# Kernel tuning notes

Measured on AMD Instinct MI355X. Metric: run time of the kernel, lower is better.

Reference implementation:

```python
import jax, jax.numpy as jnp
import numpy as np
import math

N = 4096      # n_history
D = 512       # embed_dim
H = 8         # time-weight MLP hidden size


def setup_inputs() -> dict:
    key = jax.random.key(0)
    k1, k2, k3, k4, k5 = jax.random.split(key, 5)
    return {
        "query_code_embeds": jax.random.normal(k1, (N, D), dtype=jnp.float32),
        "hist_embeddings": jax.random.normal(k2, (N, D), dtype=jnp.float32),
        "hist_times": jax.random.uniform(k3, (N,), dtype=jnp.float32),
        "tw_w1": jax.random.normal(k4, (1, H), dtype=jnp.float32) * (1.0 / math.sqrt(1.0)),
        "tw_b1": jnp.zeros((H,), dtype=jnp.float32),
        "tw_w2": jax.random.normal(k5, (H, 1), dtype=jnp.float32) * (1.0 / math.sqrt(H)),
        "tw_b2": jnp.zeros((1,), dtype=jnp.float32),
    }


def reference(query_code_embeds, hist_embeddings, hist_times, tw_w1, tw_b1, tw_w2, tw_b2):
    # pairwise absolute time differences: [n, n, 1]
    time_diffs = jnp.abs(hist_times[:, None] - hist_times[None, :])[..., None]
    # pointwise MLP on time diffs -> multiplicative attention bias [n, n]
    h = jax.nn.relu(time_diffs @ tw_w1 + tw_b1)            # [n, n, H]
    time_weights = jax.nn.sigmoid(h @ tw_w2 + tw_b2)[..., 0]  # [n, n]
    # scaled dot-product scores modulated by time weights
    scores = (query_code_embeds @ hist_embeddings.T) / math.sqrt(D)
    scores = scores * time_weights
    attn = jax.nn.softmax(scores, axis=1)
    return attn @ hist_embeddings
```

## Files before the change

### kernel.cpp

```cpp
#include <hip/hip_runtime.h>
#include <hip/hip_cooperative_groups.h>

namespace cg = cooperative_groups;

#define N 4096
#define D 512
#define FRAG_SH 512
#define NBLK 512
#define NTHR 256
#define SC_STRIDE 136
#define SMEM_BYTES 69632

typedef __attribute__((ext_vector_type(8))) short short8;
typedef __attribute__((ext_vector_type(4))) float f32x4;

__device__ __forceinline__ unsigned short f2bf(float f) {
    unsigned int u = __float_as_uint(f);
    u = (u + 0x7FFFu + ((u >> 16) & 1u)) >> 16;
    return (unsigned short)u;
}
__device__ __forceinline__ unsigned short f2bf_rn(float f) {
    return (unsigned short)((__float_as_uint(f) + 0x8000u) >> 16);
}
__device__ __forceinline__ float bf2f(unsigned short u) {
    return __uint_as_float((unsigned)u << 16);
}

__device__ __forceinline__ void prep_phase(int bid, int tid,
    const float* __restrict__ q, const float* __restrict__ hist,
    unsigned short* __restrict__ Qblk, unsigned short* __restrict__ Kblk,
    unsigned short* __restrict__ Vblk, float* __restrict__ dsum)
{
    extern __shared__ unsigned short smem[];
    if (bid >= 256) {
        if (bid < 258) {
            int z = (bid - 256) * NTHR + tid;
            #pragma unroll
            for (int j = 0; j < 8; ++j) dsum[z * 8 + j] = 0.f;
        }
        return;
    }
    const bool isQ = bid < 128;
    const int t = isQ ? bid : bid - 128;
    const float* src = isQ ? q : hist;
    const float scale = isQ ? 0.04419417382415922f : 1.0f;

    #pragma unroll
    for (int k = 0; k < 16; ++k) {
        int idx = tid + k * 256;
        int row = idx >> 7;
        int c4  = (idx & 127) << 2;
        float4 v = *(const float4*)(src + (size_t)(t * 32 + row) * D + c4);
        ushort4 o;
        o.x = f2bf(v.x * scale); o.y = f2bf(v.y * scale);
        o.z = f2bf(v.z * scale); o.w = f2bf(v.w * scale);
        *(ushort4*)(smem + row * 512 + c4) = o;
    }
    __syncthreads();

    unsigned short* ABdst = isQ ? Qblk : Kblk;
    #pragma unroll
    for (int k = 0; k < 8; ++k) {
        int s = tid + k * 256;
        int fl = s >> 6, ln = s & 63;
        int dk = fl >> 1, rbl = fl & 1;
        int l16 = ln & 15, qq = ln >> 4;
        short8 v = *(const short8*)(smem + (rbl * 16 + l16) * 512 + dk * 32 + qq * 8);
        *(short8*)(ABdst + ((size_t)dk * 256 + t * 2 + rbl) * FRAG_SH + ln * 8) = v;
    }
    if (!isQ) {
        #pragma unroll
        for (int k = 0; k < 8; ++k) {
            int s = tid + k * 256;
            int db = s >> 6, ln = s & 63;
            int l16 = ln & 15, qq = ln >> 4;
            unsigned short tmp[8];
            #pragma unroll
            for (int j = 0; j < 8; ++j)
                tmp[j] = smem[(qq * 8 + j) * 512 + db * 16 + l16];
            *(short8*)(Vblk + ((size_t)t * 32 + db) * FRAG_SH + ln * 8) = *(const short8*)tmp;
        }
    }
}

__device__ __forceinline__ void qk_phase(int bid, int tid,
    const unsigned short* __restrict__ Qblk, const unsigned short* __restrict__ Kblk,
    const float* __restrict__ times,
    const float* __restrict__ w1, const float* __restrict__ b1,
    const float* __restrict__ w2, const float* __restrict__ b2,
    unsigned short* __restrict__ Pblk, float* __restrict__ dsum)
{
    extern __shared__ unsigned short smem[];
    const int wv = tid >> 6, lane = tid & 63;
    const int qq = lane >> 4, l16 = lane & 15;
    const int wy = wv >> 1, wx = wv & 1;
    const int rg = bid >> 4;
    const int cg = bid & 15;

    f32x4 acc[4][8];
    #pragma unroll
    for (int fy = 0; fy < 4; ++fy)
        #pragma unroll
        for (int fx = 0; fx < 8; ++fx) acc[fy][fx] = (f32x4){0.f, 0.f, 0.f, 0.f};

    for (int dk = 0; dk < 16; ++dk) {
        short8 a[4], b[8];
        #pragma unroll
        for (int fy = 0; fy < 4; ++fy)
            a[fy] = *(const short8*)(Qblk + ((size_t)dk * 256 + rg * 8 + wy * 4 + fy) * FRAG_SH + lane * 8);
        #pragma unroll
        for (int fx = 0; fx < 8; ++fx)
            b[fx] = *(const short8*)(Kblk + ((size_t)dk * 256 + cg * 16 + wx * 8 + fx) * FRAG_SH + lane * 8);
        #pragma unroll
        for (int fy = 0; fy < 4; ++fy)
            #pragma unroll
            for (int fx = 0; fx < 8; ++fx)
                acc[fy][fx] = __builtin_amdgcn_mfma_f32_16x16x32_bf16(a[fy], b[fx], acc[fy][fx], 0, 0, 0);
    }

    float w1v[8], b1v[8], w2v[8];
    #pragma unroll
    for (int k = 0; k < 8; ++k) { w1v[k] = w1[k]; b1v[k] = b1[k]; w2v[k] = w2[k]; }
    const float b2v = b2[0];
    bool fast = true;
    #pragma unroll
    for (int k = 0; k < 8; ++k) fast = fast && (b1v[k] == 0.0f);
    float C1 = 0.0f;
    #pragma unroll
    for (int k = 0; k < 8; ++k) C1 += w2v[k] * fmaxf(w1v[k], 0.0f);

    const int rowbase = rg * 128 + wy * 64;
    const int colbase = cg * 256 + wx * 128;
    float tcol[8];
    #pragma unroll
    for (int fx = 0; fx < 8; ++fx) tcol[fx] = times[colbase + fx * 16 + l16];

    unsigned short* sc = smem + wv * (64 * SC_STRIDE);
    #pragma unroll
    for (int fy = 0; fy < 4; ++fy) {
        #pragma unroll
        for (int ri = 0; ri < 4; ++ri) {
            const float tq = times[rowbase + fy * 16 + qq * 4 + ri];
            float se = 0.f;
            #pragma unroll
            for (int fx = 0; fx < 8; ++fx) {
                float td = fabsf(tq - tcol[fx]);
                float a = fmaf(td, C1, b2v);
                if (!fast) {
                    a = b2v;
                    #pragma unroll
                    for (int k = 0; k < 8; ++k)
                        a += w2v[k] * fmaxf(fmaf(td, w1v[k], b1v[k]), 0.f);
                }
                float twt = __builtin_amdgcn_rcpf(1.0f + __expf(-a));
                float e = __expf(acc[fy][fx][ri] * twt);
                se += e;
                sc[(fy * 16 + qq * 4 + ri) * SC_STRIDE + fx * 16 + l16] = f2bf_rn(e);
            }
            se += __shfl_xor(se, 1);
            se += __shfl_xor(se, 2);
            se += __shfl_xor(se, 4);
            se += __shfl_xor(se, 8);
            if (l16 == 0) atomicAdd(dsum + rowbase + fy * 16 + qq * 4 + ri, se);
        }
    }
    #pragma unroll
    for (int fy = 0; fy < 4; ++fy)
        #pragma unroll
        for (int kb = 0; kb < 4; ++kb) {
            short8 v = *(const short8*)(sc + (fy * 16 + l16) * SC_STRIDE + kb * 32 + qq * 8);
            size_t fidx = (size_t)(cg * 8 + wx * 4 + kb) * 256 + (rg * 8 + wy * 4 + fy);
            *(short8*)(Pblk + fidx * FRAG_SH + lane * 8) = v;
        }
}

__device__ __forceinline__ void pv_phase(int bid, int tid,
    const unsigned short* __restrict__ Pblk, const unsigned short* __restrict__ Vblk,
    unsigned short* __restrict__ Opart, int KS2)
{
    const int wv = tid >> 6, lane = tid & 63;
    const int qq = lane >> 4, l16 = lane & 15;
    const int wy = wv >> 1, wx = wv & 1;
    const int iters = (N / 32) / KS2;
    const int units = 64 * KS2;

    for (int u = bid; u < units; u += NBLK) {
        const int chunk = u % KS2;
        const int v2 = u / KS2;
        const int cgp = v2 & 1;
        const int rg  = v2 >> 1;
        const int kbase = chunk * iters;

        f32x4 acc[4][8];
        #pragma unroll
        for (int fy = 0; fy < 4; ++fy)
            #pragma unroll
            for (int fx = 0; fx < 8; ++fx) acc[fy][fx] = (f32x4){0.f, 0.f, 0.f, 0.f};

        for (int it = 0; it < iters; ++it) {
            const int kb32 = kbase + it;
            short8 a[4], b[8];
            #pragma unroll
            for (int fy = 0; fy < 4; ++fy)
                a[fy] = *(const short8*)(Pblk + ((size_t)kb32 * 256 + rg * 8 + wy * 4 + fy) * FRAG_SH + lane * 8);
            #pragma unroll
            for (int fx = 0; fx < 8; ++fx)
                b[fx] = *(const short8*)(Vblk + ((size_t)kb32 * 32 + cgp * 16 + wx * 8 + fx) * FRAG_SH + lane * 8);
            #pragma unroll
            for (int fy = 0; fy < 4; ++fy)
                #pragma unroll
                for (int fx = 0; fx < 8; ++fx)
                    acc[fy][fx] = __builtin_amdgcn_mfma_f32_16x16x32_bf16(a[fy], b[fx], acc[fy][fx], 0, 0, 0);
        }

        unsigned short* ob = Opart + (size_t)chunk * N * D;
        #pragma unroll
        for (int fy = 0; fy < 4; ++fy)
            #pragma unroll
            for (int ri = 0; ri < 4; ++ri) {
                const int row = rg * 128 + wy * 64 + fy * 16 + qq * 4 + ri;
                #pragma unroll
                for (int fx = 0; fx < 8; ++fx) {
                    const int col = cgp * 256 + wx * 128 + fx * 16 + l16;
                    ob[(size_t)row * D + col] = f2bf_rn(acc[fy][fx][ri]);
                }
            }
    }
}

__device__ __forceinline__ void reduce_phase(int bid, int tid,
    const unsigned short* __restrict__ Opart, const float* __restrict__ dsum,
    float* __restrict__ out, int KS2)
{
    const int ND4 = N * D / 4;
    for (int i = bid * NTHR + tid; i < ND4; i += NBLK * NTHR) {
        int row = i >> 7;
        float inv = 1.0f / dsum[row];
        float4 acc = {0.f, 0.f, 0.f, 0.f};
        for (int c = 0; c < KS2; ++c) {
            ushort4 u = ((const ushort4*)(Opart + (size_t)c * N * D))[i];
            acc.x += bf2f(u.x); acc.y += bf2f(u.y);
            acc.z += bf2f(u.z); acc.w += bf2f(u.w);
        }
        acc.x *= inv; acc.y *= inv; acc.z *= inv; acc.w *= inv;
        ((float4*)out)[i] = acc;
    }
}

__global__ __launch_bounds__(NTHR, 2) void fused_kernel(
    const float* q, const float* hist, const float* times,
    const float* w1, const float* b1, const float* w2, const float* b2,
    unsigned short* Qblk, unsigned short* Kblk, unsigned short* Vblk,
    unsigned short* Pblk, float* dsum, unsigned short* Opart, float* out, int KS2)
{
    cg::grid_group grid = cg::this_grid();
    const int bid = blockIdx.x, tid = threadIdx.x;

    prep_phase(bid, tid, q, hist, Qblk, Kblk, Vblk, dsum);
    __threadfence();
    grid.sync();
    qk_phase(bid, tid, Qblk, Kblk, times, w1, b1, w2, b2, Pblk, dsum);
    __threadfence();
    grid.sync();
    pv_phase(bid, tid, Pblk, Vblk, Opart, KS2);
    __threadfence();
    grid.sync();
    reduce_phase(bid, tid, Opart, dsum, out, KS2);
}

__global__ __launch_bounds__(NTHR, 2) void prep_wrap(
    const float* q, const float* hist, unsigned short* Qblk,
    unsigned short* Kblk, unsigned short* Vblk, float* dsum)
{ prep_phase(blockIdx.x, threadIdx.x, q, hist, Qblk, Kblk, Vblk, dsum); }

__global__ __launch_bounds__(NTHR, 2) void qk_wrap(
    const unsigned short* Qblk, const unsigned short* Kblk, const float* times,
    const float* w1, const float* b1, const float* w2, const float* b2,
    unsigned short* Pblk, float* dsum)
{ qk_phase(blockIdx.x, threadIdx.x, Qblk, Kblk, times, w1, b1, w2, b2, Pblk, dsum); }

__global__ __launch_bounds__(NTHR, 2) void pv_wrap(
    const unsigned short* Pblk, const unsigned short* Vblk,
    unsigned short* Opart, int KS2)
{ pv_phase(blockIdx.x, threadIdx.x, Pblk, Vblk, Opart, KS2); }

__global__ __launch_bounds__(NTHR, 2) void reduce_wrap(
    const unsigned short* Opart, const float* dsum, float* out, int KS2)
{ reduce_phase(blockIdx.x, threadIdx.x, Opart, dsum, out, KS2); }

extern "C" void kernel_launch(void* const* d_in, const int* in_sizes, int n_in,
                              void* d_out, int out_size, void* d_ws, size_t ws_size,
                              hipStream_t stream) {
    const float* q     = (const float*)d_in[0];
    const float* hist  = (const float*)d_in[1];
    const float* times = (const float*)d_in[2];
    const float* w1    = (const float*)d_in[3];
    const float* b1    = (const float*)d_in[4];
    const float* w2    = (const float*)d_in[5];
    const float* b2    = (const float*)d_in[6];
    float* out = (float*)d_out;

    char* base = (char*)d_ws;
    const size_t MB4 = (size_t)N * D * 2;
    unsigned short* Vblk = (unsigned short*)base;
    unsigned short* Pblk = (unsigned short*)(base + MB4);
    float* dsum          = (float*)(base + MB4 + (size_t)N * (size_t)N * 2);
    char* ob             = base + MB4 + (size_t)N * (size_t)N * 2 + 65536;
    unsigned short* Qblk = (unsigned short*)ob;
    unsigned short* Kblk = (unsigned short*)(ob + MB4);
    unsigned short* Opart = (unsigned short*)ob;
    const size_t fixed = (size_t)(ob - base);
    int KS2 = (ws_size >= fixed + 8 * MB4) ? 8 :
              (ws_size >= fixed + 4 * MB4) ? 4 : 2;

    hipFuncSetAttribute((const void*)fused_kernel,
                        hipFuncAttributeMaxDynamicSharedMemorySize, SMEM_BYTES);
    hipFuncSetAttribute((const void*)qk_wrap,
                        hipFuncAttributeMaxDynamicSharedMemorySize, SMEM_BYTES);
    hipFuncSetAttribute((const void*)prep_wrap,
                        hipFuncAttributeMaxDynamicSharedMemorySize, SMEM_BYTES);

    int occ = 0;
    hipOccupancyMaxActiveBlocksPerMultiprocessor(&occ, (const void*)fused_kernel,
                                                 NTHR, SMEM_BYTES);
    if (occ >= 2) {
        void* args[] = {
            (void*)&q, (void*)&hist, (void*)&times, (void*)&w1, (void*)&b1,
            (void*)&w2, (void*)&b2, (void*)&Qblk, (void*)&Kblk, (void*)&Vblk,
            (void*)&Pblk, (void*)&dsum, (void*)&Opart, (void*)&out, (void*)&KS2
        };
        hipError_t e = hipLaunchCooperativeKernel((void*)fused_kernel,
                                                  dim3(NBLK), dim3(NTHR),
                                                  args, SMEM_BYTES, stream);
        if (e == hipSuccess) return;
        (void)hipGetLastError();
    }

    prep_wrap<<<NBLK, NTHR, 32768, stream>>>(q, hist, Qblk, Kblk, Vblk, dsum);
    qk_wrap<<<NBLK, NTHR, SMEM_BYTES, stream>>>(Qblk, Kblk, times, w1, b1, w2, b2, Pblk, dsum);
    pv_wrap<<<NBLK, NTHR, 0, stream>>>(Pblk, Vblk, Opart, KS2);
    reduce_wrap<<<NBLK, NTHR, 0, stream>>>(Opart, dsum, out, KS2);
}
```

Measured before the change: 150.6 us.

## Replace cooperative grid-sync kernel with four separate launches and retiled PV

Drops the cooperative fused kernel and its grid-wide barriers in favour of four ordinary kernel launches, each sized to its own work (258 prep blocks, 512 QK blocks, KS2x128 PV blocks, full-size reduce grid). The PV stage is retiled from 128x256 output tiles per block to 32x512 tiles, which gives more blocks and smaller per-wave accumulators. The QK block-to-column mapping is also permuted, presumably to improve cache locality across concurrently running blocks. The cost is extra launch gaps between stages, and the smaller PV tiles reuse each loaded tile less.

```diff
diff --git a/kernel.cpp b/kernel.cpp
--- a/kernel.cpp
+++ b/kernel.cpp
@@ -1,12 +1,8 @@
 #include <hip/hip_runtime.h>
-#include <hip/hip_cooperative_groups.h>
-
-namespace cg = cooperative_groups;
 
 #define N 4096
 #define D 512
 #define FRAG_SH 512
-#define NBLK 512
 #define NTHR 256
 #define SC_STRIDE 136
 #define SMEM_BYTES 69632
@@ -26,18 +22,17 @@
     return __uint_as_float((unsigned)u << 16);
 }
 
-__device__ __forceinline__ void prep_phase(int bid, int tid,
+__global__ __launch_bounds__(NTHR) void prep_kernel(
     const float* __restrict__ q, const float* __restrict__ hist,
     unsigned short* __restrict__ Qblk, unsigned short* __restrict__ Kblk,
     unsigned short* __restrict__ Vblk, float* __restrict__ dsum)
 {
-    extern __shared__ unsigned short smem[];
+    __shared__ unsigned short smem[32 * 512];
+    const int bid = blockIdx.x, tid = threadIdx.x;
     if (bid >= 256) {
-        if (bid < 258) {
-            int z = (bid - 256) * NTHR + tid;
-            #pragma unroll
-            for (int j = 0; j < 8; ++j) dsum[z * 8 + j] = 0.f;
-        }
+        int z = (bid - 256) * NTHR + tid;
+        #pragma unroll
+        for (int j = 0; j < 8; ++j) dsum[z * 8 + j] = 0.f;
         return;
     }
     const bool isQ = bid < 128;
@@ -83,7 +78,7 @@
     }
 }
 
-__device__ __forceinline__ void qk_phase(int bid, int tid,
+__global__ __launch_bounds__(NTHR, 2) void qk_kernel(
     const unsigned short* __restrict__ Qblk, const unsigned short* __restrict__ Kblk,
     const float* __restrict__ times,
     const float* __restrict__ w1, const float* __restrict__ b1,
@@ -91,11 +86,12 @@
     unsigned short* __restrict__ Pblk, float* __restrict__ dsum)
 {
     extern __shared__ unsigned short smem[];
+    const int tid = threadIdx.x, bid = blockIdx.x;
     const int wv = tid >> 6, lane = tid & 63;
     const int qq = lane >> 4, l16 = lane & 15;
     const int wy = wv >> 1, wx = wv & 1;
+    const int cg = ((bid & 7) << 1) | ((bid >> 3) & 1);
     const int rg = bid >> 4;
-    const int cg = bid & 15;
 
     f32x4 acc[4][8];
     #pragma unroll
@@ -174,119 +170,69 @@
         }
 }
 
-__device__ __forceinline__ void pv_phase(int bid, int tid,
+__global__ __launch_bounds__(NTHR, 2) void pv_kernel(
     const unsigned short* __restrict__ Pblk, const unsigned short* __restrict__ Vblk,
-    unsigned short* __restrict__ Opart, int KS2)
-{
+    unsigned short* __restrict__ Opart, int iters)
+{
+    const int tid = threadIdx.x;
     const int wv = tid >> 6, lane = tid & 63;
     const int qq = lane >> 4, l16 = lane & 15;
-    const int wy = wv >> 1, wx = wv & 1;
-    const int iters = (N / 32) / KS2;
-    const int units = 64 * KS2;
-
-    for (int u = bid; u < units; u += NBLK) {
-        const int chunk = u % KS2;
-        const int v2 = u / KS2;
-        const int cgp = v2 & 1;
-        const int rg  = v2 >> 1;
-        const int kbase = chunk * iters;
-
-        f32x4 acc[4][8];
-        #pragma unroll
-        for (int fy = 0; fy < 4; ++fy)
-            #pragma unroll
-            for (int fx = 0; fx < 8; ++fx) acc[fy][fx] = (f32x4){0.f, 0.f, 0.f, 0.f};
-
-        for (int it = 0; it < iters; ++it) {
-            const int kb32 = kbase + it;
-            short8 a[4], b[8];
-            #pragma unroll
-            for (int fy = 0; fy < 4; ++fy)
-                a[fy] = *(const short8*)(Pblk + ((size_t)kb32 * 256 + rg * 8 + wy * 4 + fy) * FRAG_SH + lane * 8);
+    const int chunk = blockIdx.x;
+    const int rg = blockIdx.y;
+    const int kbase = chunk * iters;
+
+    f32x4 acc[2][8];
+    #pragma unroll
+    for (int fy = 0; fy < 2; ++fy)
+        #pragma unroll
+        for (int fx = 0; fx < 8; ++fx) acc[fy][fx] = (f32x4){0.f, 0.f, 0.f, 0.f};
+
+    for (int it = 0; it < iters; ++it) {
+        const int kb32 = kbase + it;
+        short8 a[2], b[8];
+        #pragma unroll
+        for (int fy = 0; fy < 2; ++fy)
+            a[fy] = *(const short8*)(Pblk + ((size_t)kb32 * 256 + rg * 2 + fy) * FRAG_SH + lane * 8);
+        #pragma unroll
+        for (int fx = 0; fx < 8; ++fx)
+            b[fx] = *(const short8*)(Vblk + ((size_t)kb32 * 32 + wv * 8 + fx) * FRAG_SH + lane * 8);
+        #pragma unroll
+        for (int fy = 0; fy < 2; ++fy)
             #pragma unroll
             for (int fx = 0; fx < 8; ++fx)
-                b[fx] = *(const short8*)(Vblk + ((size_t)kb32 * 32 + cgp * 16 + wx * 8 + fx) * FRAG_SH + lane * 8);
-            #pragma unroll
-            for (int fy = 0; fy < 4; ++fy)
-                #pragma unroll
-                for (int fx = 0; fx < 8; ++fx)
-                    acc[fy][fx] = __builtin_amdgcn_mfma_f32_16x16x32_bf16(a[fy], b[fx], acc[fy][fx], 0, 0, 0);
-        }
-
-        unsigned short* ob = Opart + (size_t)chunk * N * D;
-        #pragma unroll
-        for (int fy = 0; fy < 4; ++fy)
-            #pragma unroll
-            for (int ri = 0; ri < 4; ++ri) {
-                const int row = rg * 128 + wy * 64 + fy * 16 + qq * 4 + ri;
-                #pragma unroll
-                for (int fx = 0; fx < 8; ++fx) {
-                    const int col = cgp * 256 + wx * 128 + fx * 16 + l16;
-                    ob[(size_t)row * D + col] = f2bf_rn(acc[fy][fx][ri]);
-                }
+                acc[fy][fx] = __builtin_amdgcn_mfma_f32_16x16x32_bf16(a[fy], b[fx], acc[fy][fx], 0, 0, 0);
+    }
+
+    unsigned short* ob = Opart + (size_t)chunk * N * D;
+    #pragma unroll
+    for (int fy = 0; fy < 2; ++fy)
+        #pragma unroll
+        for (int ri = 0; ri < 4; ++ri) {
+            const int row = rg * 32 + fy * 16 + qq * 4 + ri;
+            #pragma unroll
+            for (int fx = 0; fx < 8; ++fx) {
+                const int col = wv * 128 + fx * 16 + l16;
+                ob[(size_t)row * D + col] = f2bf_rn(acc[fy][fx][ri]);
             }
-    }
-}
-
-__device__ __forceinline__ void reduce_phase(int bid, int tid,
+        }
+}
+
+__global__ __launch_bounds__(NTHR) void reduce_kernel(
     const unsigned short* __restrict__ Opart, const float* __restrict__ dsum,
     float* __restrict__ out, int KS2)
 {
-    const int ND4 = N * D / 4;
-    for (int i = bid * NTHR + tid; i < ND4; i += NBLK * NTHR) {
-        int row = i >> 7;
-        float inv = 1.0f / dsum[row];
-        float4 acc = {0.f, 0.f, 0.f, 0.f};
-        for (int c = 0; c < KS2; ++c) {
-            ushort4 u = ((const ushort4*)(Opart + (size_t)c * N * D))[i];
-            acc.x += bf2f(u.x); acc.y += bf2f(u.y);
-            acc.z += bf2f(u.z); acc.w += bf2f(u.w);
-        }
-        acc.x *= inv; acc.y *= inv; acc.z *= inv; acc.w *= inv;
-        ((float4*)out)[i] = acc;
-    }
-}
-
-__global__ __launch_bounds__(NTHR, 2) void fused_kernel(
-    const float* q, const float* hist, const float* times,
-    const float* w1, const float* b1, const float* w2, const float* b2,
-    unsigned short* Qblk, unsigned short* Kblk, unsigned short* Vblk,
-    unsigned short* Pblk, float* dsum, unsigned short* Opart, float* out, int KS2)
-{
-    cg::grid_group grid = cg::this_grid();
-    const int bid = blockIdx.x, tid = threadIdx.x;
-
-    prep_phase(bid, tid, q, hist, Qblk, Kblk, Vblk, dsum);
-    __threadfence();
-    grid.sync();
-    qk_phase(bid, tid, Qblk, Kblk, times, w1, b1, w2, b2, Pblk, dsum);
-    __threadfence();
-    grid.sync();
-    pv_phase(bid, tid, Pblk, Vblk, Opart, KS2);
-    __threadfence();
-    grid.sync();
-    reduce_phase(bid, tid, Opart, dsum, out, KS2);
-}
-
-__global__ __launch_bounds__(NTHR, 2) void prep_wrap(
-    const float* q, const float* hist, unsigned short* Qblk,
-    unsigned short* Kblk, unsigned short* Vblk, float* dsum)
-{ prep_phase(blockIdx.x, threadIdx.x, q, hist, Qblk, Kblk, Vblk, dsum); }
-
-__global__ __launch_bounds__(NTHR, 2) void qk_wrap(
-    const unsigned short* Qblk, const unsigned short* Kblk, const float* times,
-    const float* w1, const float* b1, const float* w2, const float* b2,
-    unsigned short* Pblk, float* dsum)
-{ qk_phase(blockIdx.x, threadIdx.x, Qblk, Kblk, times, w1, b1, w2, b2, Pblk, dsum); }
-
-__global__ __launch_bounds__(NTHR, 2) void pv_wrap(
-    const unsigned short* Pblk, const unsigned short* Vblk,
-    unsigned short* Opart, int KS2)
-{ pv_phase(blockIdx.x, threadIdx.x, Pblk, Vblk, Opart, KS2); }
-
-__global__ __launch_bounds__(NTHR, 2) void reduce_wrap(
-    const unsigned short* Opart, const float* dsum, float* out, int KS2)
-{ reduce_phase(blockIdx.x, threadIdx.x, Opart, dsum, out, KS2); }
+    int i = blockIdx.x * NTHR + threadIdx.x;
+    int row = i >> 7;
+    float inv = 1.0f / dsum[row];
+    float4 acc = {0.f, 0.f, 0.f, 0.f};
+    for (int c = 0; c < KS2; ++c) {
+        ushort4 u = ((const ushort4*)(Opart + (size_t)c * N * D))[i];
+        acc.x += bf2f(u.x); acc.y += bf2f(u.y);
+        acc.z += bf2f(u.z); acc.w += bf2f(u.w);
+    }
+    acc.x *= inv; acc.y *= inv; acc.z *= inv; acc.w *= inv;
+    ((float4*)out)[i] = acc;
+}
 
 extern "C" void kernel_launch(void* const* d_in, const int* in_sizes, int n_in,
                               void* d_out, int out_size, void* d_ws, size_t ws_size,
@@ -310,34 +256,15 @@
     unsigned short* Kblk = (unsigned short*)(ob + MB4);
     unsigned short* Opart = (unsigned short*)ob;
     const size_t fixed = (size_t)(ob - base);
-    int KS2 = (ws_size >= fixed + 8 * MB4) ? 8 :
-              (ws_size >= fixed + 4 * MB4) ? 4 : 2;
-
-    hipFuncSetAttribute((const void*)fused_kernel,
+    const int KS2 = (ws_size >= fixed + 8 * MB4) ? 8 :
+                    (ws_size >= fixed + 4 * MB4) ? 4 : 2;
+    const int iters = (N / 32) / KS2;
+
+    hipFuncSetAttribute((const void*)qk_kernel,
                         hipFuncAttributeMaxDynamicSharedMemorySize, SMEM_BYTES);
-    hipFuncSetAttribute((const void*)qk_wrap,
-                        hipFuncAttributeMaxDynamicSharedMemorySize, SMEM_BYTES);
-    hipFuncSetAttribute((const void*)prep_wrap,
-                        hipFuncAttributeMaxDynamicSharedMemorySize, SMEM_BYTES);
-
-    int occ = 0;
-    hipOccupancyMaxActiveBlocksPerMultiprocessor(&occ, (const void*)fused_kernel,
-                                                 NTHR, SMEM_BYTES);
-    if (occ >= 2) {
-        void* args[] = {
-            (void*)&q, (void*)&hist, (void*)&times, (void*)&w1, (void*)&b1,
-            (void*)&w2, (void*)&b2, (void*)&Qblk, (void*)&Kblk, (void*)&Vblk,
-            (void*)&Pblk, (void*)&dsum, (void*)&Opart, (void*)&out, (void*)&KS2
-        };
-        hipError_t e = hipLaunchCooperativeKernel((void*)fused_kernel,
-                                                  dim3(NBLK), dim3(NTHR),
-                                                  args, SMEM_BYTES, stream);
-        if (e == hipSuccess) return;
-        (void)hipGetLastError();
-    }
-
-    prep_wrap<<<NBLK, NTHR, 32768, stream>>>(q, hist, Qblk, Kblk, Vblk, dsum);
-    qk_wrap<<<NBLK, NTHR, SMEM_BYTES, stream>>>(Qblk, Kblk, times, w1, b1, w2, b2, Pblk, dsum);
-    pv_wrap<<<NBLK, NTHR, 0, stream>>>(Pblk, Vblk, Opart, KS2);
-    reduce_wrap<<<NBLK, NTHR, 0, stream>>>(Opart, dsum, out, KS2);
-}
+
+    prep_kernel<<<258, NTHR, 0, stream>>>(q, hist, Qblk, Kblk, Vblk, dsum);
+    qk_kernel<<<512, NTHR, SMEM_BYTES, stream>>>(Qblk, Kblk, times, w1, b1, w2, b2, Pblk, dsum);
+    pv_kernel<<<dim3(KS2, 128), NTHR, 0, stream>>>(Pblk, Vblk, Opart, iters);
+    reduce_kernel<<<(N * D / 4) / NTHR, NTHR, 0, stream>>>(Opart, dsum, out, KS2);
+}
```

Result: no change. 150.1 us (-0.3%).
